# Kernel tuning notes

Hardware: AMD Instinct MI355X
Metric: run time of the kernel (lower is better)

## Reference

```python
import jax, jax.numpy as jnp
import numpy as np

N = 50000       # nodes per side (all node sets share N so concat along dim 1 works)
E = 500000      # edges per relation
B = 64          # graphs for global_mean_pool
C = 32          # per-layer hidden (latent_dim = (32,32) x10)
D = 288         # sum(latent_dim[1:,0]) = 9*32
NUM_CLASSES = 10
NUM_LAYERS = 9


def _tconv(x_s, x_d, ei, Wq, bq, Wk, bk, Wv, bv, Ws, bs, edge_feat=None, We=None):
    """PyG TransformerConv: heads=1, concat=True, beta=False, root_weight=True."""
    q = x_d @ Wq + bq                       # [Nd, C]
    k = x_s @ Wk + bk                       # [Ns, C]
    v = x_s @ Wv + bv                       # [Ns, C]
    src, dst = ei[0], ei[1]
    ke = k[src]                             # gather per edge [E, C]
    ve = v[src]
    if We is not None:                      # lin_edge (bias=False); added to key AND value
        e = edge_feat @ We
        ke = ke + e
        ve = ve + e
    nd = x_d.shape[0]
    logits = jnp.sum(q[dst] * ke, axis=-1) / jnp.sqrt(jnp.float32(C))
    m = jax.ops.segment_max(logits, dst, num_segments=nd)      # segment softmax
    ex = jnp.exp(logits - m[dst])
    denom = jax.ops.segment_sum(ex, dst, num_segments=nd)
    alpha = ex / (denom[dst] + 1e-16)
    agg = jax.ops.segment_sum(ve * alpha[:, None], dst, num_segments=nd)
    return agg + x_d @ Ws + bs              # root/skip linear (lin_skip)


def _forward(inter_emb, edge_attr, uv_target_emb,
             inter_index, uv_target_index, target_uv_index, batch,
             conv_Wq, conv_bq, conv_Wk, conv_bk, conv_Wv, conv_bv,
             conv_Ws, conv_bs, conv_We,
             lin_W1, lin_b1, lin_W2, lin_b2, lin_W3, lin_b3,
             lin_W4, lin_b4, lin_W5, lin_b5, lin_W6, lin_b6):
    f0, f1 = jnp.split(inter_emb, 2, axis=1)            # torch.chunk(x, 2, dim=1)
    edge_feat = jnp.tile(edge_attr[:, None], (1, C))    # at.reshape(-1,1).repeat(1,C)
    states = []
    x = None
    for i in range(NUM_LAYERS):
        p = (conv_Wq[i], conv_bq[i], conv_Wk[i], conv_bk[i],
             conv_Wv[i], conv_bv[i], conv_Ws[i], conv_bs[i])
        if i % 3 == 0:
            xs, xd = (f0, f1) if i == 0 else (x, x)
            x = jnp.tanh(_tconv(xs, xd, inter_index, *p, edge_feat, conv_We[i // 3]))
        elif i % 3 == 1:
            x = jnp.tanh(_tconv(x, uv_target_emb, uv_target_index, *p))
        else:
            x = jnp.tanh(_tconv(uv_target_emb, x, target_uv_index, *p))
        states.append(x)
    h = jnp.concatenate(states, axis=1) @ lin_W1 + lin_b1        # [N, 288]
    sums = jax.ops.segment_sum(h, batch, num_segments=B)
    cnt = jax.ops.segment_sum(jnp.ones((h.shape[0],), h.dtype), batch, num_segments=B)
    pooled = sums / jnp.maximum(cnt, 1.0)[:, None]               # global_mean_pool
    h = jax.nn.relu(pooled @ lin_W2 + lin_b2)
    h = h @ lin_W3 + lin_b3
    h = h @ lin_W4 + lin_b4
    h = h @ lin_W5 + lin_b5
    h = h @ lin_W6 + lin_b6
    return jax.nn.log_softmax(h, axis=-1)                        # [B, NUM_CLASSES]


def setup_inputs():
    key = jax.random.key(0)
    ks = iter(jax.random.split(key, 64))
    def nrm(shape, scale=1.0):
        return jax.random.normal(next(ks), shape, dtype=jnp.float32) * jnp.float32(scale)
    s = 1.0 / np.sqrt(C)
    inp = {
        "inter_emb": nrm((N, 2 * C)),
        "edge_attr": nrm((E,)),
        "uv_target_emb": nrm((N, C)),
        "inter_index": jax.random.randint(next(ks), (2, E), 0, N, dtype=jnp.int32),
        "uv_target_index": jax.random.randint(next(ks), (2, E), 0, N, dtype=jnp.int32),
        "target_uv_index": jax.random.randint(next(ks), (2, E), 0, N, dtype=jnp.int32),
        "batch": jnp.sort(jax.random.randint(next(ks), (N,), 0, B, dtype=jnp.int32)),
        "conv_Wq": nrm((NUM_LAYERS, C, C), s), "conv_bq": nrm((NUM_LAYERS, C), 0.01),
        "conv_Wk": nrm((NUM_LAYERS, C, C), s), "conv_bk": nrm((NUM_LAYERS, C), 0.01),
        "conv_Wv": nrm((NUM_LAYERS, C, C), s), "conv_bv": nrm((NUM_LAYERS, C), 0.01),
        "conv_Ws": nrm((NUM_LAYERS, C, C), s), "conv_bs": nrm((NUM_LAYERS, C), 0.01),
        "conv_We": nrm((3, C, C), s),
        "lin_W1": nrm((D, D), 1.0 / np.sqrt(D)), "lin_b1": nrm((D,), 0.01),
        "lin_W2": nrm((D, D // 2), 1.0 / np.sqrt(D)), "lin_b2": nrm((D // 2,), 0.01),
        "lin_W3": nrm((D // 2, D // 2), 1.0 / np.sqrt(D // 2)), "lin_b3": nrm((D // 2,), 0.01),
        "lin_W4": nrm((D // 2, D // 4), 1.0 / np.sqrt(D // 2)), "lin_b4": nrm((D // 4,), 0.01),
        "lin_W5": nrm((D // 4, D // 4), 1.0 / np.sqrt(D // 4)), "lin_b5": nrm((D // 4,), 0.01),
        "lin_W6": nrm((D // 4, NUM_CLASSES), 1.0 / np.sqrt(D // 4)), "lin_b6": nrm((NUM_CLASSES,), 0.01),
    }
    return inp


def reference(inter_emb, edge_attr, uv_target_emb,
              inter_index, uv_target_index, target_uv_index, batch,
              conv_Wq, conv_bq, conv_Wk, conv_bk, conv_Wv, conv_bv,
              conv_Ws, conv_bs, conv_We,
              lin_W1, lin_b1, lin_W2, lin_b2, lin_W3, lin_b3,
              lin_W4, lin_b4, lin_W5, lin_b5, lin_W6, lin_b6):
    return _forward(inter_emb, edge_attr, uv_target_emb,
                    inter_index, uv_target_index, target_uv_index, batch,
                    conv_Wq, conv_bq, conv_Wk, conv_bk, conv_Wv, conv_bv,
                    conv_Ws, conv_bs, conv_We,
                    lin_W1, lin_b1, lin_W2, lin_b2, lin_W3, lin_b3,
                    lin_W4, lin_b4, lin_W5, lin_b5, lin_W6, lin_b6)
```

## Files before the change

### kernel.cpp

```cpp
#include <hip/hip_runtime.h>
#include <hip/hip_fp16.h>
#include <math.h>

#define RSQRT32 0.17677669529663687f
#define NS 8
#define NC 32
#define MAXBS 6336
#define TILE 2048

typedef float fx2 __attribute__((ext_vector_type(2)));


__global__ void hist_lds(const int* __restrict__ e0, const int* __restrict__ e1,
                         const int* __restrict__ e2, int E, int N, int BS, int CH,
                         unsigned short* __restrict__ partial) {
    __shared__ unsigned int h[MAXBS];
    int blk = blockIdx.x;
    int c = blk % NC, s = (blk / NC) % NS, r = blk / (NC * NS);
    int lo = s * BS, hi = min(lo + BS, N), nb = hi - lo;
    for (int i = threadIdx.x; i < nb; i += 256) h[i] = 0;
    __syncthreads();
    const int* ei = (r == 0) ? e0 : ((r == 1) ? e1 : e2);
    int ebeg = c * CH, eend = min(ebeg + CH, E);
    const int* dst = ei + E;
    for (int i = ebeg + (int)threadIdx.x; i < eend; i += 256) {
        int d = dst[i];
        if (d >= lo && d < hi) atomicAdd(&h[d - lo], 1u);
    }
    __syncthreads();
    unsigned short* out = partial + ((size_t)blk) * BS;
    for (int i = threadIdx.x; i < nb; i += 256) out[i] = (unsigned short)h[i];
}

__global__ void chunk_scan(unsigned short* __restrict__ partial, int* __restrict__ cnt3,
                           int N, int BS) {
    int t = blockIdx.x * blockDim.x + threadIdx.x;
    int tot = 3 * NS * BS;
    if (t >= tot) return;
    int r = t / (NS * BS);
    int rem = t - r * NS * BS;
    int s = rem / BS, bin = rem - s * BS;
    int d = s * BS + bin;
    if (d >= N) return;
    size_t base = ((size_t)(r * NS + s) * NC) * BS + bin;
    unsigned int run = 0;
    for (int c = 0; c < NC; ++c) {
        unsigned int v = partial[base + (size_t)c * BS];
        partial[base + (size_t)c * BS] = (unsigned short)run;
        run += v;
    }
    cnt3[(size_t)r * N + d] = (int)run;
}

__global__ void scan_tiles_sum(const int* __restrict__ cnt3, int* __restrict__ tsum,
                               int N, int G) {
    int blk = blockIdx.x, r = blk / G, g = blk - r * G;
    int base = g * TILE;
    const int* cnt = cnt3 + (size_t)r * N;
    int s = 0;
    for (int i = threadIdx.x; i < TILE; i += 256) {
        int idx = base + i;
        s += (idx < N) ? cnt[idx] : 0;
    }
    __shared__ int wsum[4];
    for (int m = 32; m; m >>= 1) s += __shfl_down(s, m);
    if ((threadIdx.x & 63) == 0) wsum[threadIdx.x >> 6] = s;
    __syncthreads();
    if (threadIdx.x == 0) tsum[blk] = wsum[0] + wsum[1] + wsum[2] + wsum[3];
}

__global__ void scan_offsets(int* __restrict__ tsum, int* __restrict__ rp3, int N, int G) {
    int r = threadIdx.x;
    if (r < 3) {
        int run = 0;
        for (int g = 0; g < G; ++g) { int v = tsum[r * G + g]; tsum[r * G + g] = run; run += v; }
        rp3[(size_t)r * (N + 1) + N] = run;
    }
}

__global__ void scan_write(const int* __restrict__ cnt3, const int* __restrict__ toff,
                           int* __restrict__ rp3, int N, int G) {
    int blk = blockIdx.x, r = blk / G, g = blk - r * G;
    int base = g * TILE;
    const int* cnt = cnt3 + (size_t)r * N;
    int* rp = rp3 + (size_t)r * (N + 1);
    __shared__ int part[256];
    int t = threadIdx.x;
    int v[8]; int s = 0;
    #pragma unroll
    for (int j = 0; j < 8; ++j) {
        int idx = base + t * 8 + j;
        int x = (idx < N) ? cnt[idx] : 0;
        v[j] = s; s += x;
    }
    part[t] = s;
    __syncthreads();
    for (int off = 1; off < 256; off <<= 1) {
        int x = (t >= off) ? part[t - off] : 0;
        __syncthreads();
        part[t] += x;
        __syncthreads();
    }
    int texcl = part[t] - s + toff[blk];
    #pragma unroll
    for (int j = 0; j < 8; ++j) {
        int idx = base + t * 8 + j;
        if (idx < N) rp[idx] = texcl + v[j];
    }
}

__global__ void scatter_cs(const int* __restrict__ e0, const int* __restrict__ e1,
                           const int* __restrict__ e2, const float* __restrict__ ea,
                           const unsigned short* __restrict__ partial,
                           const int* __restrict__ rp3,
                           int2* __restrict__ adj0, int* __restrict__ adj12,
                           int E, int N, int BS, int CH) {
    __shared__ unsigned int cur[MAXBS];
    int blk = blockIdx.x;
    int s = blk & 7;
    int rest = blk >> 3;
    int c = rest % NC, r = rest / NC;
    int pblk = c + NC * (s + NS * r);
    int lo = s * BS, hi = min(lo + BS, N), nb = hi - lo;
    const unsigned short* po = partial + ((size_t)pblk) * BS;
    const int* rp = rp3 + (size_t)r * (N + 1);
    for (int i = threadIdx.x; i < nb; i += 256)
        cur[i] = (unsigned int)rp[lo + i] + (unsigned int)po[i];
    __syncthreads();
    const int* ei = (r == 0) ? e0 : ((r == 1) ? e1 : e2);
    const int* srcp = ei;
    const int* dstp = ei + E;
    int ebeg = c * CH, eend = min(ebeg + CH, E);
    if (r == 0) {
        for (int i = ebeg + (int)threadIdx.x; i < eend; i += 256) {
            int d = dstp[i];
            if (d < lo || d >= hi) continue;
            unsigned int pos = atomicAdd(&cur[d - lo], 1u);
            int2 v; v.x = srcp[i]; v.y = __float_as_int(ea[i]);
            adj0[pos] = v;
        }
    } else {
        int* adj = adj12 + (size_t)(r - 1) * E;
        for (int i = ebeg + (int)threadIdx.x; i < eend; i += 256) {
            int d = dstp[i];
            if (d < lo || d >= hi) continue;
            unsigned int pos = atomicAdd(&cur[d - lo], 1u);
            adj[pos] = srcp[i];
        }
    }
}


__global__ void colsum_kernel(const float* __restrict__ We, float* __restrict__ u) {
    int t = threadIdx.x;
    if (t < 96) {
        int w = t >> 5, j = t & 31;
        const float* W = We + w * 1024;
        float s = 0.f;
        #pragma unroll
        for (int kk = 0; kk < 32; ++kk) s += W[kk * 32 + j];
        u[t] = s;
    }
}

__global__ void bounds_kernel(const int* __restrict__ batch, int* __restrict__ bstart,
                              int* __restrict__ bend, int N) {
    int t = blockIdx.x * blockDim.x + threadIdx.x;
    if (t >= N) return;
    int b = batch[t];
    if (t == 0 || batch[t - 1] != b) bstart[b] = t;
    if (t == N - 1 || batch[t + 1] != b) bend[b] = t + 1;
}

__global__ void qkvs_kernel(
    const float* __restrict__ xs, int ssrc,
    const float* __restrict__ xd, int sdst,
    const float* __restrict__ Wq, const float* __restrict__ bq,
    const float* __restrict__ Wk, const float* __restrict__ bk,
    const float* __restrict__ Wv, const float* __restrict__ bv,
    const float* __restrict__ Ws, const float* __restrict__ bs,
    const float* __restrict__ u,
    float* __restrict__ qb, uint2* __restrict__ kv8,
    float* __restrict__ sb, float* __restrict__ qdu, int N)
{
    int lane = threadIdx.x & 63;
    int wid  = __builtin_amdgcn_readfirstlane((int)(threadIdx.x >> 6));
    int wpb  = blockDim.x >> 6;
    int gw   = blockIdx.x * wpb + wid;
    int nw   = gridDim.x * wpb;
    int j    = lane & 31;
    bool lower = lane < 32;

    const float* W1 = lower ? Wq : Wk;
    const float* W2 = lower ? Wv : Ws;
    float rw1[32], rw2[32];
    #pragma unroll
    for (int kk = 0; kk < 32; ++kk) {
        rw1[kk] = W1[kk * 32 + j];
        rw2[kk] = W2[kk * 32 + j];
    }
    float bias1 = lower ? bq[j] : bk[j];
    float bias2 = lower ? bv[j] : bs[j];
    float uj = (u != nullptr) ? u[j] : 0.f;

    for (int n = gw; n < N; n += nw) {
        const float* xdr = xd + (size_t)n * sdst;
        const float* xsr = xs + (size_t)n * ssrc;
        float acc1 = bias1, acc2 = bias2;
        #pragma unroll
        for (int kk = 0; kk < 32; ++kk) {
            float xdv = xdr[kk];
            float xsv = xsr[kk];
            float a  = lower ? xdv : xsv;
            float bb = lower ? xsv : xdv;
            acc1 = fmaf(a,  rw1[kk], acc1);
            acc2 = fmaf(bb, rw2[kk], acc2);
        }
        float kk_ = __shfl(acc1, j + 32);
        float k1 = __shfl_down(kk_, 1), v1 = __shfl_down(acc2, 1);
        float k2 = __shfl_down(kk_, 2), v2 = __shfl_down(acc2, 2);
        float k3 = __shfl_down(kk_, 3), v3 = __shfl_down(acc2, 3);
        if (lower) {
            qb[(size_t)n * 32 + j] = acc1;
            if ((j & 3) == 0) {
                int pk = __builtin_amdgcn_cvt_pk_fp8_f32(kk_, k1, 0, false);
                pk = __builtin_amdgcn_cvt_pk_fp8_f32(k2, k3, pk, true);
                int pv = __builtin_amdgcn_cvt_pk_fp8_f32(acc2, v1, 0, false);
                pv = __builtin_amdgcn_cvt_pk_fp8_f32(v2, v3, pv, true);
                kv8[(size_t)n * 8 + (j >> 2)] = make_uint2((unsigned)pk, (unsigned)pv);
            }
        } else {
            sb[(size_t)n * 32 + j] = acc2;
        }
        if (u != nullptr) {
            float pp = lower ? acc1 * uj : 0.f;
            pp += __shfl_xor(pp, 16);
            pp += __shfl_xor(pp, 8);
            pp += __shfl_xor(pp, 4);
            pp += __shfl_xor(pp, 2);
            pp += __shfl_xor(pp, 1);
            if (lane == 0) qdu[n] = pp * RSQRT32;
        }
    }
}

template<int HAS_EA>
__global__ __launch_bounds__(256, 8)
void agg_kernel(const int* __restrict__ rp, const void* __restrict__ adjv,
    const float* __restrict__ qb, const uint2* __restrict__ kv8,
    const float* __restrict__ qdu, const float* __restrict__ u,
    const float* __restrict__ skp, float* __restrict__ xout, int N)
{
    int t = threadIdx.x;
    int w = t >> 6, lane = t & 63;
    int cq = lane & 7;
    int o  = lane >> 3;
    int n = blockIdx.x * 4 + w;
    if (n >= N) return;
    float4 qc = ((const float4*)(qb + (size_t)n * 32))[cq];
    float qd = HAS_EA ? qdu[n] : 0.f;
    float4 uc = HAS_EA ? ((const float4*)u)[cq] : make_float4(0.f, 0.f, 0.f, 0.f);
    int beg = rp[n], end = rp[n + 1];
    float den0 = 0.f, den1 = 0.f;
    float4 num0 = make_float4(0.f, 0.f, 0.f, 0.f);
    float4 num1 = make_float4(0.f, 0.f, 0.f, 0.f);
    const int2* adjE = (const int2*)adjv;
    const int*  adjP = (const int*)adjv;
    int i = beg + o;
    for (; i + 8 < end; i += 16) {
        int s0, s1; float ae0 = 0.f, ae1 = 0.f;
        if (HAS_EA) {
            int2 a0 = adjE[i], a1 = adjE[i + 8];
            s0 = a0.x; s1 = a1.x;
            ae0 = __int_as_float(a0.y); ae1 = __int_as_float(a1.y);
        } else { s0 = adjP[i]; s1 = adjP[i + 8]; }
        uint2 p0 = kv8[(size_t)s0 * 8 + cq];
        uint2 p1 = kv8[(size_t)s1 * 8 + cq];
        fx2 k001 = __builtin_amdgcn_cvt_pk_f32_fp8((int)p0.x, false);
        fx2 k023 = __builtin_amdgcn_cvt_pk_f32_fp8((int)p0.x, true);
        fx2 w001 = __builtin_amdgcn_cvt_pk_f32_fp8((int)p0.y, false);
        fx2 w023 = __builtin_amdgcn_cvt_pk_f32_fp8((int)p0.y, true);
        fx2 k101 = __builtin_amdgcn_cvt_pk_f32_fp8((int)p1.x, false);
        fx2 k123 = __builtin_amdgcn_cvt_pk_f32_fp8((int)p1.x, true);
        fx2 w101 = __builtin_amdgcn_cvt_pk_f32_fp8((int)p1.y, false);
        fx2 w123 = __builtin_amdgcn_cvt_pk_f32_fp8((int)p1.y, true);
        float d0 = fmaf(qc.x, k001[0], fmaf(qc.y, k001[1], fmaf(qc.z, k023[0], qc.w * k023[1])));
        float d1 = fmaf(qc.x, k101[0], fmaf(qc.y, k101[1], fmaf(qc.z, k123[0], qc.w * k123[1])));
        d0 += __shfl_xor(d0, 4);  d1 += __shfl_xor(d1, 4);
        d0 += __shfl_xor(d0, 2);  d1 += __shfl_xor(d1, 2);
        d0 += __shfl_xor(d0, 1);  d1 += __shfl_xor(d1, 1);
        float ex0 = __expf(fmaf(ae0, qd, d0 * RSQRT32));
        float ex1 = __expf(fmaf(ae1, qd, d1 * RSQRT32));
        den0 += ex0;  den1 += ex1;
        num0.x = fmaf(fmaf(ae0, uc.x, w001[0]), ex0, num0.x);
        num0.y = fmaf(fmaf(ae0, uc.y, w001[1]), ex0, num0.y);
        num0.z = fmaf(fmaf(ae0, uc.z, w023[0]), ex0, num0.z);
        num0.w = fmaf(fmaf(ae0, uc.w, w023[1]), ex0, num0.w);
        num1.x = fmaf(fmaf(ae1, uc.x, w101[0]), ex1, num1.x);
        num1.y = fmaf(fmaf(ae1, uc.y, w101[1]), ex1, num1.y);
        num1.z = fmaf(fmaf(ae1, uc.z, w123[0]), ex1, num1.z);
        num1.w = fmaf(fmaf(ae1, uc.w, w123[1]), ex1, num1.w);
    }
    for (; i < end; i += 8) {
        int s0; float ae0 = 0.f;
        if (HAS_EA) { int2 a0 = adjE[i]; s0 = a0.x; ae0 = __int_as_float(a0.y); }
        else s0 = adjP[i];
        uint2 p0 = kv8[(size_t)s0 * 8 + cq];
        fx2 k001 = __builtin_amdgcn_cvt_pk_f32_fp8((int)p0.x, false);
        fx2 k023 = __builtin_amdgcn_cvt_pk_f32_fp8((int)p0.x, true);
        fx2 w001 = __builtin_amdgcn_cvt_pk_f32_fp8((int)p0.y, false);
        fx2 w023 = __builtin_amdgcn_cvt_pk_f32_fp8((int)p0.y, true);
        float d0 = fmaf(qc.x, k001[0], fmaf(qc.y, k001[1], fmaf(qc.z, k023[0], qc.w * k023[1])));
        d0 += __shfl_xor(d0, 4);
        d0 += __shfl_xor(d0, 2);
        d0 += __shfl_xor(d0, 1);
        float ex0 = __expf(fmaf(ae0, qd, d0 * RSQRT32));
        den0 += ex0;
        num0.x = fmaf(fmaf(ae0, uc.x, w001[0]), ex0, num0.x);
        num0.y = fmaf(fmaf(ae0, uc.y, w001[1]), ex0, num0.y);
        num0.z = fmaf(fmaf(ae0, uc.z, w023[0]), ex0, num0.z);
        num0.w = fmaf(fmaf(ae0, uc.w, w023[1]), ex0, num0.w);
    }
    float den = den0 + den1;
    float4 num = make_float4(num0.x + num1.x, num0.y + num1.y,
                             num0.z + num1.z, num0.w + num1.w);
    den   += __shfl_xor(den, 8);   den   += __shfl_xor(den, 16);   den   += __shfl_xor(den, 32);
    num.x += __shfl_xor(num.x, 8); num.x += __shfl_xor(num.x, 16); num.x += __shfl_xor(num.x, 32);
    num.y += __shfl_xor(num.y, 8); num.y += __shfl_xor(num.y, 16); num.y += __shfl_xor(num.y, 32);
    num.z += __shfl_xor(num.z, 8); num.z += __shfl_xor(num.z, 16); num.z += __shfl_xor(num.z, 32);
    num.w += __shfl_xor(num.w, 8); num.w += __shfl_xor(num.w, 16); num.w += __shfl_xor(num.w, 32);
    if (o == 0) {
        float inv = 1.f / (den + 1e-16f);
        float4 sk = ((const float4*)(skp + (size_t)n * 32))[cq];
        float4 ov;
        ov.x = tanhf(fmaf(num.x, inv, sk.x));
        ov.y = tanhf(fmaf(num.y, inv, sk.y));
        ov.z = tanhf(fmaf(num.z, inv, sk.z));
        ov.w = tanhf(fmaf(num.w, inv, sk.w));
        ((float4*)(xout + (size_t)n * 32))[cq] = ov;
    }
}

__global__ void pool_kernel(const float* __restrict__ x,
                            const int* __restrict__ bstart, const int* __restrict__ bend,
                            float* __restrict__ poolsum, int layer_off) {
    __shared__ float red[256];
    int b = blockIdx.x >> 3, sub = blockIdx.x & 7;
    int s0 = bstart[b], s1 = bend[b];
    int cnt = s1 - s0;
    int n0 = s0 + (int)((long long)cnt * sub / 8);
    int n1 = s0 + (int)((long long)cnt * (sub + 1) / 8);
    int t = threadIdx.x, col = t & 31, g = t >> 5;
    float acc = 0.f;
    for (int n = n0 + g; n < n1; n += 8)
        acc += x[(size_t)n * 32 + col];
    red[t] = acc;
    __syncthreads();
    if (t < 32) {
        float s = red[t];
        #pragma unroll
        for (int k = 1; k < 8; ++k) s += red[t + 32 * k];
        atomicAdd(&poolsum[(size_t)b * 288 + layer_off + t], s);
    }
}


__device__ __forceinline__ void gemv_step(const float* __restrict__ W, const float* __restrict__ bias,
    const float* sin_, float* sout, int K, int M, int t, bool do_relu) {
    if (t < M) {
        float acc = bias[t];
        for (int kk = 0; kk < K; ++kk) acc = fmaf(sin_[kk], W[kk * M + t], acc);
        sout[t] = do_relu ? fmaxf(acc, 0.f) : acc;
    }
    __syncthreads();
}

__global__ void head_kernel(const float* __restrict__ poolsum,
    const int* __restrict__ bstart, const int* __restrict__ bend,
    const float* __restrict__ W1, const float* __restrict__ b1,
    const float* __restrict__ W2, const float* __restrict__ b2,
    const float* __restrict__ W3, const float* __restrict__ b3,
    const float* __restrict__ W4, const float* __restrict__ b4,
    const float* __restrict__ W5, const float* __restrict__ b5,
    const float* __restrict__ W6, const float* __restrict__ b6,
    float* __restrict__ out)
{
    __shared__ float ha[288], hb[288];
    __shared__ float lse;
    int b = blockIdx.x, t = threadIdx.x;
    float invc = 1.f / fmaxf((float)(bend[b] - bstart[b]), 1.f);
    if (t < 288) ha[t] = poolsum[(size_t)b * 288 + t] * invc;
    __syncthreads();
    gemv_step(W1, b1, ha, hb, 288, 288, t, false);
    gemv_step(W2, b2, hb, ha, 288, 144, t, true);
    gemv_step(W3, b3, ha, hb, 144, 144, t, false);
    gemv_step(W4, b4, hb, ha, 144, 72,  t, false);
    gemv_step(W5, b5, ha, hb, 72,  72,  t, false);
    gemv_step(W6, b6, hb, ha, 72,  10,  t, false);
    if (t == 0) {
        float m = ha[0];
        for (int i = 1; i < 10; ++i) m = fmaxf(m, ha[i]);
        float ssum = 0.f;
        for (int i = 0; i < 10; ++i) ssum += __expf(ha[i] - m);
        lse = m + logf(ssum);
    }
    __syncthreads();
    if (t < 10) out[b * 10 + t] = ha[t] - lse;
}


extern "C" void kernel_launch(void* const* d_in, const int* in_sizes, int n_in,
                              void* d_out, int out_size, void* d_ws, size_t ws_size,
                              hipStream_t stream)
{
    const float* inter_emb = (const float*)d_in[0];
    const float* edge_attr = (const float*)d_in[1];
    const float* uv_emb    = (const float*)d_in[2];
    const int* inter_idx = (const int*)d_in[3];
    const int* uvt_idx   = (const int*)d_in[4];
    const int* tuv_idx   = (const int*)d_in[5];
    const int* batch     = (const int*)d_in[6];
    const float* cWq = (const float*)d_in[7];  const float* cbq = (const float*)d_in[8];
    const float* cWk = (const float*)d_in[9];  const float* cbk = (const float*)d_in[10];
    const float* cWv = (const float*)d_in[11]; const float* cbv = (const float*)d_in[12];
    const float* cWs = (const float*)d_in[13]; const float* cbs = (const float*)d_in[14];
    const float* cWe = (const float*)d_in[15];
    const float* W1 = (const float*)d_in[16]; const float* b1 = (const float*)d_in[17];
    const float* W2 = (const float*)d_in[18]; const float* b2 = (const float*)d_in[19];
    const float* W3 = (const float*)d_in[20]; const float* b3 = (const float*)d_in[21];
    const float* W4 = (const float*)d_in[22]; const float* b4 = (const float*)d_in[23];
    const float* W5 = (const float*)d_in[24]; const float* b5 = (const float*)d_in[25];
    const float* W6 = (const float*)d_in[26]; const float* b6 = (const float*)d_in[27];

    const int N = in_sizes[2] / 32;
    const int E = in_sizes[1];
    const int B = out_size / 10;
    const int G = (N + TILE - 1) / TILE;
    const int BS = (N + NS - 1) / NS;
    const int CH = (E + NC - 1) / NC;

    char* p = (char*)d_ws;
    auto alloc = [&](size_t bytes) { char* r = p; p += (bytes + 255) & ~(size_t)255; return r; };
    float*   qb    = (float*)alloc((size_t)N * 32 * 4);
    uint2*   kv8   = (uint2*)alloc((size_t)N * 64);
    float*   sb    = (float*)alloc((size_t)N * 32 * 4);
    float*   qdu   = (float*)alloc((size_t)N * 4);
    float*   xa    = (float*)alloc((size_t)N * 32 * 4);
    float*   xb    = (float*)alloc((size_t)N * 32 * 4);
    float*   ub    = (float*)alloc(96 * 4);
    float*   poolsum = (float*)alloc((size_t)B * 288 * 4);
    int*     bstart = (int*)alloc((size_t)B * 4);
    int*     bend   = (int*)alloc((size_t)B * 4);
    int*     cnt3  = (int*)alloc((size_t)3 * N * 4);
    int*     rp3   = (int*)alloc((size_t)3 * (N + 1) * 4);
    int*     tsum  = (int*)alloc((size_t)3 * G * 4);
    unsigned short* partial = (unsigned short*)alloc((size_t)3 * NS * NC * BS * 2);
    int2*    adj0  = (int2*)alloc((size_t)E * 8);
    int*     adj12 = (int*)alloc((size_t)2 * E * 4);

    hist_lds<<<3 * NS * NC, 256, 0, stream>>>(inter_idx, uvt_idx, tuv_idx, E, N, BS, CH, partial);
    chunk_scan<<<(3 * NS * BS + 255) / 256, 256, 0, stream>>>(partial, cnt3, N, BS);
    scan_tiles_sum<<<3 * G, 256, 0, stream>>>(cnt3, tsum, N, G);
    scan_offsets<<<1, 64, 0, stream>>>(tsum, rp3, N, G);
    scan_write<<<3 * G, 256, 0, stream>>>(cnt3, tsum, rp3, N, G);
    scatter_cs<<<3 * NS * NC, 256, 0, stream>>>(inter_idx, uvt_idx, tuv_idx, edge_attr,
                                                partial, rp3, adj0, adj12, E, N, BS, CH);

    hipMemsetAsync(poolsum, 0, (size_t)B * 288 * 4, stream);
    hipMemsetAsync(bstart, 0, (size_t)B * 4, stream);
    hipMemsetAsync(bend, 0, (size_t)B * 4, stream);
    colsum_kernel<<<1, 128, 0, stream>>>(cWe, ub);
    bounds_kernel<<<(N + 255) / 256, 256, 0, stream>>>(batch, bstart, bend, N);

    float* xcur = nullptr;
    float* xnext = xa;
    for (int i = 0; i < 9; ++i) {
        int r = i % 3;
        const float* xsrc; int ssrc; const float* xdst; int sdst;
        if (i == 0)      { xsrc = inter_emb; ssrc = 64; xdst = inter_emb + 32; sdst = 64; }
        else if (r == 0) { xsrc = xcur; ssrc = 32; xdst = xcur;  sdst = 32; }
        else if (r == 1) { xsrc = xcur; ssrc = 32; xdst = uv_emb; sdst = 32; }
        else             { xsrc = uv_emb; ssrc = 32; xdst = xcur; sdst = 32; }
        const float* ul = (r == 0) ? (ub + (i / 3) * 32) : nullptr;

        qkvs_kernel<<<1024, 256, 0, stream>>>(xsrc, ssrc, xdst, sdst,
            cWq + i * 1024, cbq + i * 32, cWk + i * 1024, cbk + i * 32,
            cWv + i * 1024, cbv + i * 32, cWs + i * 1024, cbs + i * 32,
            ul, qb, kv8, sb, qdu, N);
        const int* rpl = rp3 + (size_t)r * (N + 1);
        if (r == 0) {
            agg_kernel<1><<<(N + 3) / 4, 256, 0, stream>>>(
                rpl, adj0, qb, kv8, qdu, ul, sb, xnext, N);
        } else {
            agg_kernel<0><<<(N + 3) / 4, 256, 0, stream>>>(
                rpl, adj12 + (size_t)(r - 1) * E, qb, kv8, qdu, ul, sb, xnext, N);
        }
        pool_kernel<<<B * 8, 256, 0, stream>>>(xnext, bstart, bend, poolsum, i * 32);
        xcur = xnext;
        xnext = (xnext == xa) ? xb : xa;
    }

    head_kernel<<<B, 320, 0, stream>>>(poolsum, bstart, bend,
        W1, b1, W2, b2, W3, b3, W4, b4, W5, b5, W6, b6, (float*)d_out);
}
```

Measured before the change: 627.7 us.

## Fuse global mean-pool accumulation into aggregation kernel epilogue

Removes the separate pool kernel per layer. Each aggregation block now reduces its four node outputs in LDS and atomically adds them into the per-graph pooled sums, falling back to per-node atomics when a block spans two graphs. The bstart/bend memsets are also folded into the colsum kernel. This saves nine launches and the re-read of x, but adds a __syncthreads and many more global atomics (about 12.5k blocks × 32 per layer) contending on 64×32 addresses.

```diff
diff --git a/kernel.cpp b/kernel.cpp
--- a/kernel.cpp
+++ b/kernel.cpp
@@ -151,7 +151,8 @@
 }
 
 
-__global__ void colsum_kernel(const float* __restrict__ We, float* __restrict__ u) {
+__global__ void colsum_kernel(const float* __restrict__ We, float* __restrict__ u,
+                              int* __restrict__ bstart, int* __restrict__ bend, int B) {
     int t = threadIdx.x;
     if (t < 96) {
         int w = t >> 5, j = t & 31;
@@ -161,6 +162,7 @@
         for (int kk = 0; kk < 32; ++kk) s += W[kk * 32 + j];
         u[t] = s;
     }
+    if (t < B) { bstart[t] = 0; bend[t] = 0; }
 }
 
 __global__ void bounds_kernel(const int* __restrict__ batch, int* __restrict__ bstart,
@@ -249,118 +251,121 @@
 void agg_kernel(const int* __restrict__ rp, const void* __restrict__ adjv,
     const float* __restrict__ qb, const uint2* __restrict__ kv8,
     const float* __restrict__ qdu, const float* __restrict__ u,
-    const float* __restrict__ skp, float* __restrict__ xout, int N)
+    const float* __restrict__ skp, float* __restrict__ xout,
+    const int* __restrict__ batch, float* __restrict__ poolsum,
+    int layer_off, int N)
 {
+    __shared__ float4 red4[32];
     int t = threadIdx.x;
     int w = t >> 6, lane = t & 63;
     int cq = lane & 7;
     int o  = lane >> 3;
     int n = blockIdx.x * 4 + w;
-    if (n >= N) return;
-    float4 qc = ((const float4*)(qb + (size_t)n * 32))[cq];
-    float qd = HAS_EA ? qdu[n] : 0.f;
-    float4 uc = HAS_EA ? ((const float4*)u)[cq] : make_float4(0.f, 0.f, 0.f, 0.f);
-    int beg = rp[n], end = rp[n + 1];
-    float den0 = 0.f, den1 = 0.f;
-    float4 num0 = make_float4(0.f, 0.f, 0.f, 0.f);
-    float4 num1 = make_float4(0.f, 0.f, 0.f, 0.f);
-    const int2* adjE = (const int2*)adjv;
-    const int*  adjP = (const int*)adjv;
-    int i = beg + o;
-    for (; i + 8 < end; i += 16) {
-        int s0, s1; float ae0 = 0.f, ae1 = 0.f;
-        if (HAS_EA) {
-            int2 a0 = adjE[i], a1 = adjE[i + 8];
-            s0 = a0.x; s1 = a1.x;
-            ae0 = __int_as_float(a0.y); ae1 = __int_as_float(a1.y);
-        } else { s0 = adjP[i]; s1 = adjP[i + 8]; }
-        uint2 p0 = kv8[(size_t)s0 * 8 + cq];
-        uint2 p1 = kv8[(size_t)s1 * 8 + cq];
-        fx2 k001 = __builtin_amdgcn_cvt_pk_f32_fp8((int)p0.x, false);
-        fx2 k023 = __builtin_amdgcn_cvt_pk_f32_fp8((int)p0.x, true);
-        fx2 w001 = __builtin_amdgcn_cvt_pk_f32_fp8((int)p0.y, false);
-        fx2 w023 = __builtin_amdgcn_cvt_pk_f32_fp8((int)p0.y, true);
-        fx2 k101 = __builtin_amdgcn_cvt_pk_f32_fp8((int)p1.x, false);
-        fx2 k123 = __builtin_amdgcn_cvt_pk_f32_fp8((int)p1.x, true);
-        fx2 w101 = __builtin_amdgcn_cvt_pk_f32_fp8((int)p1.y, false);
-        fx2 w123 = __builtin_amdgcn_cvt_pk_f32_fp8((int)p1.y, true);
-        float d0 = fmaf(qc.x, k001[0], fmaf(qc.y, k001[1], fmaf(qc.z, k023[0], qc.w * k023[1])));
-        float d1 = fmaf(qc.x, k101[0], fmaf(qc.y, k101[1], fmaf(qc.z, k123[0], qc.w * k123[1])));
-        d0 += __shfl_xor(d0, 4);  d1 += __shfl_xor(d1, 4);
-        d0 += __shfl_xor(d0, 2);  d1 += __shfl_xor(d1, 2);
-        d0 += __shfl_xor(d0, 1);  d1 += __shfl_xor(d1, 1);
-        float ex0 = __expf(fmaf(ae0, qd, d0 * RSQRT32));
-        float ex1 = __expf(fmaf(ae1, qd, d1 * RSQRT32));
-        den0 += ex0;  den1 += ex1;
-        num0.x = fmaf(fmaf(ae0, uc.x, w001[0]), ex0, num0.x);
-        num0.y = fmaf(fmaf(ae0, uc.y, w001[1]), ex0, num0.y);
-        num0.z = fmaf(fmaf(ae0, uc.z, w023[0]), ex0, num0.z);
-        num0.w = fmaf(fmaf(ae0, uc.w, w023[1]), ex0, num0.w);
-        num1.x = fmaf(fmaf(ae1, uc.x, w101[0]), ex1, num1.x);
-        num1.y = fmaf(fmaf(ae1, uc.y, w101[1]), ex1, num1.y);
-        num1.z = fmaf(fmaf(ae1, uc.z, w123[0]), ex1, num1.z);
-        num1.w = fmaf(fmaf(ae1, uc.w, w123[1]), ex1, num1.w);
-    }
-    for (; i < end; i += 8) {
-        int s0; float ae0 = 0.f;
-        if (HAS_EA) { int2 a0 = adjE[i]; s0 = a0.x; ae0 = __int_as_float(a0.y); }
-        else s0 = adjP[i];
-        uint2 p0 = kv8[(size_t)s0 * 8 + cq];
-        fx2 k001 = __builtin_amdgcn_cvt_pk_f32_fp8((int)p0.x, false);
-        fx2 k023 = __builtin_amdgcn_cvt_pk_f32_fp8((int)p0.x, true);
-        fx2 w001 = __builtin_amdgcn_cvt_pk_f32_fp8((int)p0.y, false);
-        fx2 w023 = __builtin_amdgcn_cvt_pk_f32_fp8((int)p0.y, true);
-        float d0 = fmaf(qc.x, k001[0], fmaf(qc.y, k001[1], fmaf(qc.z, k023[0], qc.w * k023[1])));
-        d0 += __shfl_xor(d0, 4);
-        d0 += __shfl_xor(d0, 2);
-        d0 += __shfl_xor(d0, 1);
-        float ex0 = __expf(fmaf(ae0, qd, d0 * RSQRT32));
-        den0 += ex0;
-        num0.x = fmaf(fmaf(ae0, uc.x, w001[0]), ex0, num0.x);
-        num0.y = fmaf(fmaf(ae0, uc.y, w001[1]), ex0, num0.y);
-        num0.z = fmaf(fmaf(ae0, uc.z, w023[0]), ex0, num0.z);
-        num0.w = fmaf(fmaf(ae0, uc.w, w023[1]), ex0, num0.w);
-    }
-    float den = den0 + den1;
-    float4 num = make_float4(num0.x + num1.x, num0.y + num1.y,
-                             num0.z + num1.z, num0.w + num1.w);
-    den   += __shfl_xor(den, 8);   den   += __shfl_xor(den, 16);   den   += __shfl_xor(den, 32);
-    num.x += __shfl_xor(num.x, 8); num.x += __shfl_xor(num.x, 16); num.x += __shfl_xor(num.x, 32);
-    num.y += __shfl_xor(num.y, 8); num.y += __shfl_xor(num.y, 16); num.y += __shfl_xor(num.y, 32);
-    num.z += __shfl_xor(num.z, 8); num.z += __shfl_xor(num.z, 16); num.z += __shfl_xor(num.z, 32);
-    num.w += __shfl_xor(num.w, 8); num.w += __shfl_xor(num.w, 16); num.w += __shfl_xor(num.w, 32);
-    if (o == 0) {
-        float inv = 1.f / (den + 1e-16f);
-        float4 sk = ((const float4*)(skp + (size_t)n * 32))[cq];
-        float4 ov;
-        ov.x = tanhf(fmaf(num.x, inv, sk.x));
-        ov.y = tanhf(fmaf(num.y, inv, sk.y));
-        ov.z = tanhf(fmaf(num.z, inv, sk.z));
-        ov.w = tanhf(fmaf(num.w, inv, sk.w));
-        ((float4*)(xout + (size_t)n * 32))[cq] = ov;
-    }
-}
-
-__global__ void pool_kernel(const float* __restrict__ x,
-                            const int* __restrict__ bstart, const int* __restrict__ bend,
-                            float* __restrict__ poolsum, int layer_off) {
-    __shared__ float red[256];
-    int b = blockIdx.x >> 3, sub = blockIdx.x & 7;
-    int s0 = bstart[b], s1 = bend[b];
-    int cnt = s1 - s0;
-    int n0 = s0 + (int)((long long)cnt * sub / 8);
-    int n1 = s0 + (int)((long long)cnt * (sub + 1) / 8);
-    int t = threadIdx.x, col = t & 31, g = t >> 5;
-    float acc = 0.f;
-    for (int n = n0 + g; n < n1; n += 8)
-        acc += x[(size_t)n * 32 + col];
-    red[t] = acc;
-    __syncthreads();
-    if (t < 32) {
-        float s = red[t];
-        #pragma unroll
-        for (int k = 1; k < 8; ++k) s += red[t + 32 * k];
-        atomicAdd(&poolsum[(size_t)b * 288 + layer_off + t], s);
+    bool valid = (n < N);
+    float4 ov = make_float4(0.f, 0.f, 0.f, 0.f);
+    if (valid) {
+        float4 qc = ((const float4*)(qb + (size_t)n * 32))[cq];
+        float qd = HAS_EA ? qdu[n] : 0.f;
+        float4 uc = HAS_EA ? ((const float4*)u)[cq] : make_float4(0.f, 0.f, 0.f, 0.f);
+        int beg = rp[n], end = rp[n + 1];
+        float den0 = 0.f, den1 = 0.f;
+        float4 num0 = make_float4(0.f, 0.f, 0.f, 0.f);
+        float4 num1 = make_float4(0.f, 0.f, 0.f, 0.f);
+        const int2* adjE = (const int2*)adjv;
+        const int*  adjP = (const int*)adjv;
+        int i = beg + o;
+        for (; i + 8 < end; i += 16) {
+            int s0, s1; float ae0 = 0.f, ae1 = 0.f;
+            if (HAS_EA) {
+                int2 a0 = adjE[i], a1 = adjE[i + 8];
+                s0 = a0.x; s1 = a1.x;
+                ae0 = __int_as_float(a0.y); ae1 = __int_as_float(a1.y);
+            } else { s0 = adjP[i]; s1 = adjP[i + 8]; }
+            uint2 p0 = kv8[(size_t)s0 * 8 + cq];
+            uint2 p1 = kv8[(size_t)s1 * 8 + cq];
+            fx2 k001 = __builtin_amdgcn_cvt_pk_f32_fp8((int)p0.x, false);
+            fx2 k023 = __builtin_amdgcn_cvt_pk_f32_fp8((int)p0.x, true);
+            fx2 w001 = __builtin_amdgcn_cvt_pk_f32_fp8((int)p0.y, false);
+            fx2 w023 = __builtin_amdgcn_cvt_pk_f32_fp8((int)p0.y, true);
+            fx2 k101 = __builtin_amdgcn_cvt_pk_f32_fp8((int)p1.x, false);
+            fx2 k123 = __builtin_amdgcn_cvt_pk_f32_fp8((int)p1.x, true);
+            fx2 w101 = __builtin_amdgcn_cvt_pk_f32_fp8((int)p1.y, false);
+            fx2 w123 = __builtin_amdgcn_cvt_pk_f32_fp8((int)p1.y, true);
+            float d0 = fmaf(qc.x, k001[0], fmaf(qc.y, k001[1], fmaf(qc.z, k023[0], qc.w * k023[1])));
+            float d1 = fmaf(qc.x, k101[0], fmaf(qc.y, k101[1], fmaf(qc.z, k123[0], qc.w * k123[1])));
+            d0 += __shfl_xor(d0, 4);  d1 += __shfl_xor(d1, 4);
+            d0 += __shfl_xor(d0, 2);  d1 += __shfl_xor(d1, 2);
+            d0 += __shfl_xor(d0, 1);  d1 += __shfl_xor(d1, 1);
+            float ex0 = __expf(fmaf(ae0, qd, d0 * RSQRT32));
+            float ex1 = __expf(fmaf(ae1, qd, d1 * RSQRT32));
+            den0 += ex0;  den1 += ex1;
+            num0.x = fmaf(fmaf(ae0, uc.x, w001[0]), ex0, num0.x);
+            num0.y = fmaf(fmaf(ae0, uc.y, w001[1]), ex0, num0.y);
+            num0.z = fmaf(fmaf(ae0, uc.z, w023[0]), ex0, num0.z);
+            num0.w = fmaf(fmaf(ae0, uc.w, w023[1]), ex0, num0.w);
+            num1.x = fmaf(fmaf(ae1, uc.x, w101[0]), ex1, num1.x);
+            num1.y = fmaf(fmaf(ae1, uc.y, w101[1]), ex1, num1.y);
+            num1.z = fmaf(fmaf(ae1, uc.z, w123[0]), ex1, num1.z);
+            num1.w = fmaf(fmaf(ae1, uc.w, w123[1]), ex1, num1.w);
+        }
+        for (; i < end; i += 8) {
+            int s0; float ae0 = 0.f;
+            if (HAS_EA) { int2 a0 = adjE[i]; s0 = a0.x; ae0 = __int_as_float(a0.y); }
+            else s0 = adjP[i];
+            uint2 p0 = kv8[(size_t)s0 * 8 + cq];
+            fx2 k001 = __builtin_amdgcn_cvt_pk_f32_fp8((int)p0.x, false);
+            fx2 k023 = __builtin_amdgcn_cvt_pk_f32_fp8((int)p0.x, true);
+            fx2 w001 = __builtin_amdgcn_cvt_pk_f32_fp8((int)p0.y, false);
+            fx2 w023 = __builtin_amdgcn_cvt_pk_f32_fp8((int)p0.y, true);
+            float d0 = fmaf(qc.x, k001[0], fmaf(qc.y, k001[1], fmaf(qc.z, k023[0], qc.w * k023[1])));
+            d0 += __shfl_xor(d0, 4);
+            d0 += __shfl_xor(d0, 2);
+            d0 += __shfl_xor(d0, 1);
+            float ex0 = __expf(fmaf(ae0, qd, d0 * RSQRT32));
+            den0 += ex0;
+            num0.x = fmaf(fmaf(ae0, uc.x, w001[0]), ex0, num0.x);
+            num0.y = fmaf(fmaf(ae0, uc.y, w001[1]), ex0, num0.y);
+            num0.z = fmaf(fmaf(ae0, uc.z, w023[0]), ex0, num0.z);
+            num0.w = fmaf(fmaf(ae0, uc.w, w023[1]), ex0, num0.w);
+        }
+        float den = den0 + den1;
+        float4 num = make_float4(num0.x + num1.x, num0.y + num1.y,
+                                 num0.z + num1.z, num0.w + num1.w);
+        den   += __shfl_xor(den, 8);   den   += __shfl_xor(den, 16);   den   += __shfl_xor(den, 32);
+        num.x += __shfl_xor(num.x, 8); num.x += __shfl_xor(num.x, 16); num.x += __shfl_xor(num.x, 32);
+        num.y += __shfl_xor(num.y, 8); num.y += __shfl_xor(num.y, 16); num.y += __shfl_xor(num.y, 32);
+        num.z += __shfl_xor(num.z, 8); num.z += __shfl_xor(num.z, 16); num.z += __shfl_xor(num.z, 32);
+        num.w += __shfl_xor(num.w, 8); num.w += __shfl_xor(num.w, 16); num.w += __shfl_xor(num.w, 32);
+        if (o == 0) {
+            float inv = 1.f / (den + 1e-16f);
+            float4 sk = ((const float4*)(skp + (size_t)n * 32))[cq];
+            ov.x = tanhf(fmaf(num.x, inv, sk.x));
+            ov.y = tanhf(fmaf(num.y, inv, sk.y));
+            ov.z = tanhf(fmaf(num.z, inv, sk.z));
+            ov.w = tanhf(fmaf(num.w, inv, sk.w));
+            ((float4*)(xout + (size_t)n * 32))[cq] = ov;
+        }
+    }
+    int n0 = blockIdx.x * 4;
+    int nlast = min(n0 + 3, N - 1);
+    bool uniform = (batch[n0] == batch[nlast]);
+    if (o == 0) red4[w * 8 + cq] = ov;
+    __syncthreads();
+    if (uniform) {
+        if (t < 8) {
+            float4 s0 = red4[t], s1 = red4[t + 8], s2 = red4[t + 16], s3 = red4[t + 24];
+            float* dst = poolsum + (size_t)batch[n0] * 288 + layer_off + 4 * t;
+            atomicAdd(&dst[0], s0.x + s1.x + s2.x + s3.x);
+            atomicAdd(&dst[1], s0.y + s1.y + s2.y + s3.y);
+            atomicAdd(&dst[2], s0.z + s1.z + s2.z + s3.z);
+            atomicAdd(&dst[3], s0.w + s1.w + s2.w + s3.w);
+        }
+    } else if (valid && o == 0) {
+        float* dst = poolsum + (size_t)batch[n] * 288 + layer_off + 4 * cq;
+        atomicAdd(&dst[0], ov.x);
+        atomicAdd(&dst[1], ov.y);
+        atomicAdd(&dst[2], ov.z);
+        atomicAdd(&dst[3], ov.w);
     }
 }
 
@@ -467,9 +472,7 @@
                                                 partial, rp3, adj0, adj12, E, N, BS, CH);
 
     hipMemsetAsync(poolsum, 0, (size_t)B * 288 * 4, stream);
-    hipMemsetAsync(bstart, 0, (size_t)B * 4, stream);
-    hipMemsetAsync(bend, 0, (size_t)B * 4, stream);
-    colsum_kernel<<<1, 128, 0, stream>>>(cWe, ub);
+    colsum_kernel<<<1, 128, 0, stream>>>(cWe, ub, bstart, bend, B);
     bounds_kernel<<<(N + 255) / 256, 256, 0, stream>>>(batch, bstart, bend, N);
 
     float* xcur = nullptr;
@@ -490,12 +493,12 @@
         const int* rpl = rp3 + (size_t)r * (N + 1);
         if (r == 0) {
             agg_kernel<1><<<(N + 3) / 4, 256, 0, stream>>>(
-                rpl, adj0, qb, kv8, qdu, ul, sb, xnext, N);
+                rpl, adj0, qb, kv8, qdu, ul, sb, xnext, batch, poolsum, i * 32, N);
         } else {
             agg_kernel<0><<<(N + 3) / 4, 256, 0, stream>>>(
-                rpl, adj12 + (size_t)(r - 1) * E, qb, kv8, qdu, ul, sb, xnext, N);
-        }
-        pool_kernel<<<B * 8, 256, 0, stream>>>(xnext, bstart, bend, poolsum, i * 32);
+                rpl, adj12 + (size_t)(r - 1) * E, qb, kv8, qdu, ul, sb, xnext,
+                batch, poolsum, i * 32, N);
+        }
         xcur = xnext;
         xnext = (xnext == xa) ? xb : xa;
     }
```

Measured after the change: 848.8 us. 35.2% more time.
